# Performance work log

Hardware: AMD Instinct MI355X
Metric: run time of the kernel (lower is better)

Reference implementation:

```python
import jax, jax.numpy as jnp
import numpy as np

B, S, H, F_IN = 256, 128, 512, 1


def _lstm_step(h, c, x, Wih, Whh, b):
    # PyTorch LSTM gate order: i, f, g, o
    gates = x @ Wih.T + h @ Whh.T + b  # (B, 4H)
    i, f, g, o = jnp.split(gates, 4, axis=-1)
    c = jax.nn.sigmoid(f) * c + jax.nn.sigmoid(i) * jnp.tanh(g)
    h = jax.nn.sigmoid(o) * jnp.tanh(c)
    return h, c


def setup_inputs() -> dict:
    key = jax.random.key(0)
    ks = jax.random.split(key, 18)
    p = lambda k, shape: (jax.random.normal(k, shape, dtype=jnp.float32) * 0.05)
    return {
        "input_seq": jax.random.normal(ks[0], (B, S, F_IN), dtype=jnp.float32),
        # encoder: embedding Linear(F_IN -> H) + LSTM(H -> H)
        "We_e": p(ks[1], (H, F_IN)), "be_e": p(ks[2], (H,)),
        "Wih_e": p(ks[3], (4 * H, H)), "Whh_e": p(ks[4], (4 * H, H)), "b_e": p(ks[5], (4 * H,)),
        # decoder: embedding Linear(F_IN -> H) + LSTMCell(H -> H)
        "We_d": p(ks[6], (H, F_IN)), "be_d": p(ks[7], (H,)),
        "Wih_d": p(ks[8], (4 * H, H)), "Whh_d": p(ks[9], (4 * H, H)), "b_d": p(ks[10], (4 * H,)),
        # additive attention: W_1, W_2 (H->H), v (H->1)
        "W1": p(ks[11], (H, H)), "b1": p(ks[12], (H,)),
        "W2": p(ks[13], (H, H)), "b2": p(ks[14], (H,)),
        "v": p(ks[15], (1, H)), "bv": p(ks[16], (1,)),
    }


def reference(input_seq, We_e, be_e, Wih_e, Whh_e, b_e,
              We_d, be_d, Wih_d, Whh_d, b_d,
              W1, b1, W2, b2, v, bv):
    # ---- encoder: embed then LSTM over the sequence ----
    emb = input_seq @ We_e.T + be_e  # (B, S, H)

    def enc_step(carry, x_t):
        h, c = carry
        h, c = _lstm_step(h, c, x_t, Wih_e, Whh_e, b_e)
        return (h, c), h

    h0 = jnp.zeros((B, H), dtype=input_seq.dtype)
    (h, c), enc_h = jax.lax.scan(enc_step, (h0, h0), jnp.swapaxes(emb, 0, 1))
    encoder_output = jnp.swapaxes(enc_h, 0, 1)  # (B, S, H)

    # W_1(encoder_output) is loop-invariant; hoist it (same math as the
    # original, which redundantly recomputes it every step).
    w1enc = encoder_output @ W1.T + b1  # (B, S, H)

    # ---- decoder: per-step LSTMCell + additive attention ----
    def dec_step(carry, _):
        hd, cd, x_in = carry
        e = x_in @ We_d.T + be_d  # (B, H)
        hd, cd = _lstm_step(hd, cd, e, Wih_d, Whh_d, b_d)
        q = hd @ W2.T + b2  # (B, H)
        u = jnp.squeeze(jnp.tanh(w1enc + q[:, None, :]) @ v.T + bv, -1)  # (B, S)
        att = jax.nn.log_softmax(u, axis=1)
        idx = jnp.argmax(att, axis=1)  # pointer (B,)
        # next decoder input = pointed-to input symbol
        x_next = jnp.take_along_axis(input_seq[:, :, 0], idx[:, None], axis=1)  # (B, 1)
        return (hd, cd, x_next), (att, idx)

    x0 = jnp.zeros((B, 1), dtype=input_seq.dtype)
    _, (scores, ptrs) = jax.lax.scan(dec_step, (h, c, x0), None, length=S)
    pointers_scores = jnp.swapaxes(scores, 0, 1)  # (B, S, S) log-probs
    pointers = jnp.swapaxes(ptrs, 0, 1)  # (B, S) int
    return pointers_scores, pointers
```

## Files before the change

### kernel.cpp

```cpp
#include <hip/hip_runtime.h>
#include <hip/hip_fp16.h>

#define Bn 256
#define Sn 128
#define Hn 512
#define G4 2048
#define NBLK 256
#define NTHR 1024
#define HSTR 516
#define LOG2E 1.4426950408889634f

typedef float f4v __attribute__((ext_vector_type(4)));

__device__ __forceinline__ float sigf(float x){
    float e = expf(-fabsf(x));
    float d = 1.f + e;
    return x >= 0.f ? 1.f/d : e/d;
}
__device__ __forceinline__ float ftanh(float x){
    float e = __builtin_amdgcn_exp2f(-2.f * LOG2E * fabsf(x));
    float t = (1.f - e) * __builtin_amdgcn_rcpf(1.f + e);
    return copysignf(t, x);
}

__device__ __forceinline__ float cload(const float* p){
    return __hip_atomic_load((float*)p, __ATOMIC_RELAXED, __HIP_MEMORY_SCOPE_AGENT);
}
__device__ __forceinline__ void cstore(float* p, float v){
    __hip_atomic_store(p, v, __ATOMIC_RELAXED, __HIP_MEMORY_SCOPE_AGENT);
}
__device__ __forceinline__ f4v vload4(const float* p){
    return *(volatile const f4v*)p;
}

__device__ __forceinline__ void gbar(unsigned* slots, unsigned k, int grp){
    __syncthreads();
    if (threadIdx.x < 64) {
        if (threadIdx.x == 0)
            __hip_atomic_store(slots + grp, k, __ATOMIC_RELAXED, __HIP_MEMORY_SCOPE_AGENT);
        unsigned v = (threadIdx.x < 16)
            ? __hip_atomic_load(slots + threadIdx.x, __ATOMIC_RELAXED, __HIP_MEMORY_SCOPE_AGENT)
            : k;
        while (__ballot(v < k)) {
            __builtin_amdgcn_s_sleep(1);
            v = (threadIdx.x < 16)
                ? __hip_atomic_load(slots + threadIdx.x, __ATOMIC_RELAXED, __HIP_MEMORY_SCOPE_AGENT)
                : k;
        }
        asm volatile("" ::: "memory");
    }
    __syncthreads();
}
__device__ __forceinline__ void gbar_sys(unsigned* cnt){
    __syncthreads();
    if (threadIdx.x == 0) {
        __hip_atomic_fetch_add(cnt, 1u, __ATOMIC_RELEASE, __HIP_MEMORY_SCOPE_AGENT);
        while (__hip_atomic_load(cnt, __ATOMIC_RELAXED, __HIP_MEMORY_SCOPE_AGENT) < 16u)
            __builtin_amdgcn_s_sleep(1);
        (void)__hip_atomic_load(cnt, __ATOMIC_ACQUIRE, __HIP_MEMORY_SCOPE_AGENT);
    }
    __syncthreads();
}

__global__ void precompute_kernel(
    const float* __restrict__ Wih_e, const float* __restrict__ We_e,
    const float* __restrict__ be_e,  const float* __restrict__ b_e,
    const float* __restrict__ Wih_d, const float* __restrict__ We_d,
    const float* __restrict__ be_d,  const float* __restrict__ b_d,
    float* __restrict__ p1, float* __restrict__ p0,
    float* __restrict__ r1, float* __restrict__ r0)
{
    int j = blockIdx.x*blockDim.x + threadIdx.x;
    bool dec = j >= G4;
    int jj = dec ? j - G4 : j;
    const float* Wih = dec ? Wih_d : Wih_e;
    const float* We  = dec ? We_d  : We_e;
    const float* be  = dec ? be_d  : be_e;
    const float* bb  = dec ? b_d   : b_e;
    float s1 = 0.f, s0 = 0.f;
    for (int k = 0; k < Hn; ++k) {
        float w = Wih[jj*Hn + k];
        s1 += w * We[k];
        s0 += w * be[k];
    }
    s0 += bb[jj];
    if (dec) { r1[jj] = s1; r0[jj] = s0; }
    else     { p1[jj] = s1; p0[jj] = s0; }
}

__global__ __launch_bounds__(NTHR, 4) void ptrnet_kernel(
    const float* __restrict__ xseq,
    const float* __restrict__ Whh_e, const float* __restrict__ Whh_d,
    const float* __restrict__ W1, const float* __restrict__ b1,
    const float* __restrict__ W2, const float* __restrict__ b2,
    const float* __restrict__ vv,
    const float* __restrict__ p1, const float* __restrict__ p0,
    const float* __restrict__ r1, const float* __restrict__ r0,
    float* __restrict__ hb0, float* __restrict__ hb1,
    float* __restrict__ cbuf, float* __restrict__ qbuf,
    float* __restrict__ x_in, float* __restrict__ w1enc,
    unsigned* __restrict__ barb,
    float* __restrict__ out_scores, float* __restrict__ out_ptr)
{
    __shared__ float smem[16*HSTR + 512*5 + 16];
    float* hs  = smem;
    float* red = smem + 16*HSTR;
    float* qs  = smem;
    float* us  = smem + Hn;
    float* rr  = smem + Hn + Sn + 8;

    const int blk = blockIdx.x;
    const int tid = threadIdx.x;
    const int bt  = blk >> 4, grp = blk & 15;
    const int b0  = bt << 4;
    const int tb  = tid & 15;
    const int hh  = (tid >> 4) & 31;
    const int ks  = tid >> 9;
    const int hg  = (grp << 5) + hh;
    const int kofs = ks << 8;
    unsigned* slots  = barb + bt*64;
    unsigned* syscnt = barb + 1024 + bt*64;
    unsigned bk = 0;
    float* hprev = hb0;
    float* hnext = hb1;

    const int l64 = tid & 63;
    const int kb = l64 << 3;
    float vreg[8];
    #pragma unroll
    for (int j = 0; j < 8; ++j) vreg[j] = vv[kb+j];

#define STAGE_H(SRC) do { \
    for (int i_ = tid; i_ < 16*128; i_ += NTHR) { \
        int r_ = i_ >> 7; int c4_ = (i_ & 127) << 2; \
        *(f4v*)(hs + r_*HSTR + c4_) = vload4((SRC) + (size_t)(b0+r_)*Hn + c4_); \
    } __syncthreads(); } while(0)

    for (int t = 0; t <= Sn; ++t) {
        STAGE_H(hprev);
        float a0=0.f,a1=0.f,a2=0.f,a3=0.f,a4=0.f;
        {
            const float* hrow = hs + tb*HSTR + kofs;
            const float* w0 = Whh_e + (size_t)hg*Hn          + kofs;
            const float* w1r= Whh_e + (size_t)(Hn+hg)*Hn     + kofs;
            const float* w2r= Whh_e + (size_t)(2*Hn+hg)*Hn   + kofs;
            const float* w3r= Whh_e + (size_t)(3*Hn+hg)*Hn   + kofs;
            const float* w4r= W1    + (size_t)hg*Hn          + kofs;
            for (int i = 0; i < 256; i += 4) {
                float4 hv = *(const float4*)(hrow + i);
                float4 x0 = *(const float4*)(w0 + i);
                float4 x1 = *(const float4*)(w1r + i);
                float4 x2 = *(const float4*)(w2r + i);
                float4 x3 = *(const float4*)(w3r + i);
                float4 x4 = *(const float4*)(w4r + i);
                a0 += hv.x*x0.x + hv.y*x0.y + hv.z*x0.z + hv.w*x0.w;
                a1 += hv.x*x1.x + hv.y*x1.y + hv.z*x1.z + hv.w*x1.w;
                a2 += hv.x*x2.x + hv.y*x2.y + hv.z*x2.z + hv.w*x2.w;
                a3 += hv.x*x3.x + hv.y*x3.y + hv.z*x3.z + hv.w*x3.w;
                a4 += hv.x*x4.x + hv.y*x4.y + hv.z*x4.z + hv.w*x4.w;
            }
        }
        if (ks) {
            float* rp = red + (size_t)(tid - 512)*5;
            rp[0]=a0; rp[1]=a1; rp[2]=a2; rp[3]=a3; rp[4]=a4;
        }
        __syncthreads();
        if (!ks) {
            const float* rp = red + (size_t)tid*5;
            a0+=rp[0]; a1+=rp[1]; a2+=rp[2]; a3+=rp[3]; a4+=rp[4];
            size_t off = (size_t)(b0+tb)*Hn + hg;
            if (t < Sn) {
                float xv = xseq[(b0+tb)*Sn + t];
                float gi = a0 + xv*p1[hg]      + p0[hg];
                float gf = a1 + xv*p1[Hn+hg]   + p0[Hn+hg];
                float gg = a2 + xv*p1[2*Hn+hg] + p0[2*Hn+hg];
                float go = a3 + xv*p1[3*Hn+hg] + p0[3*Hn+hg];
                float cn = sigf(gf)*cbuf[off] + sigf(gi)*tanhf(gg);
                float hn = sigf(go)*tanhf(cn);
                cbuf[off] = cn;
                cstore(hnext + off, hn);
            }
            if (t > 0)
                w1enc[((size_t)(b0+tb)*Sn + (t-1))*Hn + hg] = a4 + b1[hg];
        }
        if (t == Sn) gbar_sys(syscnt);
        else         { ++bk; gbar(slots, bk, grp); }
        if (t < Sn) { float* tp = hprev; hprev = hnext; hnext = tp; }
    }

    for (int t = 0; t < Sn; ++t) {
        STAGE_H(hprev);
        float a0=0.f,a1=0.f,a2=0.f,a3=0.f;
        {
            const float* hrow = hs + tb*HSTR + kofs;
            const float* w0 = Whh_d + (size_t)hg*Hn        + kofs;
            const float* w1r= Whh_d + (size_t)(Hn+hg)*Hn   + kofs;
            const float* w2r= Whh_d + (size_t)(2*Hn+hg)*Hn + kofs;
            const float* w3r= Whh_d + (size_t)(3*Hn+hg)*Hn + kofs;
            for (int i = 0; i < 256; i += 4) {
                float4 hv = *(const float4*)(hrow + i);
                float4 x0 = *(const float4*)(w0 + i);
                float4 x1 = *(const float4*)(w1r + i);
                float4 x2 = *(const float4*)(w2r + i);
                float4 x3 = *(const float4*)(w3r + i);
                a0 += hv.x*x0.x + hv.y*x0.y + hv.z*x0.z + hv.w*x0.w;
                a1 += hv.x*x1.x + hv.y*x1.y + hv.z*x1.z + hv.w*x1.w;
                a2 += hv.x*x2.x + hv.y*x2.y + hv.z*x2.z + hv.w*x2.w;
                a3 += hv.x*x3.x + hv.y*x3.y + hv.z*x3.z + hv.w*x3.w;
            }
        }
        if (ks) {
            float* rp = red + (size_t)(tid - 512)*4;
            rp[0]=a0; rp[1]=a1; rp[2]=a2; rp[3]=a3;
        }
        __syncthreads();
        if (!ks) {
            const float* rp = red + (size_t)tid*4;
            a0+=rp[0]; a1+=rp[1]; a2+=rp[2]; a3+=rp[3];
            size_t off = (size_t)(b0+tb)*Hn + hg;
            float xv = cload(x_in + b0 + tb);
            float gi = a0 + xv*r1[hg]      + r0[hg];
            float gf = a1 + xv*r1[Hn+hg]   + r0[Hn+hg];
            float gg = a2 + xv*r1[2*Hn+hg] + r0[2*Hn+hg];
            float go = a3 + xv*r1[3*Hn+hg] + r0[3*Hn+hg];
            float cn = sigf(gf)*cbuf[off] + sigf(gi)*tanhf(gg);
            float hn = sigf(go)*tanhf(cn);
            cbuf[off] = cn;
            cstore(hnext + off, hn);
        }
        ++bk; gbar(slots, bk, grp);
        { float* tp = hprev; hprev = hnext; hnext = tp; }

        STAGE_H(hprev);
        float qa = 0.f;
        {
            const float* hrow = hs + tb*HSTR + kofs;
            const float* wq = W2 + (size_t)hg*Hn + kofs;
            for (int i = 0; i < 256; i += 4) {
                float4 hv = *(const float4*)(hrow + i);
                float4 wv = *(const float4*)(wq + i);
                qa += hv.x*wv.x + hv.y*wv.y + hv.z*wv.z + hv.w*wv.w;
            }
        }
        if (ks) red[tid - 512] = qa;
        __syncthreads();
        if (!ks) cstore(qbuf + (size_t)(b0+tb)*Hn + hg, qa + red[tid] + b2[hg]);
        ++bk; gbar(slots, bk, grp);

        const int b = blk;
        if (tid < 128) {
            f4v q4 = vload4(qbuf + (size_t)b*Hn + (tid << 2));
            *(f4v*)(qs + (tid << 2)) = q4;
        }
        __syncthreads();
        const int wv2 = tid >> 6;
        float qreg[8];
        #pragma unroll
        for (int j = 0; j < 8; ++j) qreg[j] = qs[kb+j];
        #pragma unroll
        for (int si = 0; si < 8; ++si) {
            const int s = (wv2 << 3) + si;
            const float* wr = w1enc + ((size_t)b*Sn + s)*Hn + kb;
            f4v w0 = *(const f4v*)wr;
            f4v w1v = *(const f4v*)(wr + 4);
            float a = 0.f;
            a += vreg[0]*ftanh(w0[0] + qreg[0]);
            a += vreg[1]*ftanh(w0[1] + qreg[1]);
            a += vreg[2]*ftanh(w0[2] + qreg[2]);
            a += vreg[3]*ftanh(w0[3] + qreg[3]);
            a += vreg[4]*ftanh(w1v[0] + qreg[4]);
            a += vreg[5]*ftanh(w1v[1] + qreg[5]);
            a += vreg[6]*ftanh(w1v[2] + qreg[6]);
            a += vreg[7]*ftanh(w1v[3] + qreg[7]);
            a += __shfl_xor(a, 1);  a += __shfl_xor(a, 2);  a += __shfl_xor(a, 4);
            a += __shfl_xor(a, 8);  a += __shfl_xor(a, 16); a += __shfl_xor(a, 32);
            if (l64 == 0) us[s] = a;
        }
        __syncthreads();
        if (tid < 64) {
            float av = us[tid], c2 = us[tid+64];
            float mv; int mi;
            if (c2 > av) { mv = c2; mi = tid+64; } else { mv = av; mi = tid; }
            #pragma unroll
            for (int off2 = 1; off2 < 64; off2 <<= 1) {
                float ov = __shfl_xor(mv, off2);
                int   oi = __shfl_xor(mi, off2);
                if (ov > mv || (ov == mv && oi < mi)) { mv = ov; mi = oi; }
            }
            float es = expf(av - mv) + expf(c2 - mv);
            #pragma unroll
            for (int off2 = 1; off2 < 64; off2 <<= 1) es += __shfl_xor(es, off2);
            if (tid == 0) {
                rr[0] = mv; rr[1] = logf(es);
                out_ptr[b*Sn + t] = (float)mi;
                cstore(x_in + b, xseq[b*Sn + mi]);
            }
        }
        __syncthreads();
        if (tid < Sn)
            out_scores[((size_t)b*Sn + t)*Sn + tid] = us[tid] - rr[0] - rr[1];
        if (t < Sn-1) { ++bk; gbar(slots, bk, grp); }
    }
#undef STAGE_H
}

extern "C" void kernel_launch(void* const* d_in, const int* in_sizes, int n_in,
                              void* d_out, int out_size, void* d_ws, size_t ws_size,
                              hipStream_t stream)
{
    const float* input_seq = (const float*)d_in[0];
    const float* We_e = (const float*)d_in[1],  *be_e = (const float*)d_in[2];
    const float* Wih_e = (const float*)d_in[3], *Whh_e = (const float*)d_in[4];
    const float* b_e = (const float*)d_in[5];
    const float* We_d = (const float*)d_in[6],  *be_d = (const float*)d_in[7];
    const float* Wih_d = (const float*)d_in[8], *Whh_d = (const float*)d_in[9];
    const float* b_d = (const float*)d_in[10];
    const float* W1 = (const float*)d_in[11], *b1 = (const float*)d_in[12];
    const float* W2 = (const float*)d_in[13], *b2 = (const float*)d_in[14];
    const float* v  = (const float*)d_in[15];

    float* ws = (float*)d_ws;
    size_t o = 0;
    float* hb0  = ws + o; o += Bn*Hn;
    float* hb1  = ws + o; o += Bn*Hn;
    float* cbuf = ws + o; o += Bn*Hn;
    float* qbuf = ws + o; o += Bn*Hn;
    float* p1   = ws + o; o += G4;
    float* p0   = ws + o; o += G4;
    float* r1   = ws + o; o += G4;
    float* r0   = ws + o; o += G4;
    float* x_in = ws + o; o += 256;
    unsigned* barb = (unsigned*)(ws + o); o += 2048;
    float* w1enc = ws + o;

    hipMemsetAsync(hb0,  0, Bn*Hn*sizeof(float), stream);
    hipMemsetAsync(cbuf, 0, Bn*Hn*sizeof(float), stream);
    hipMemsetAsync(x_in, 0, (256+2048)*sizeof(float), stream);

    precompute_kernel<<<dim3(16), 256, 0, stream>>>(Wih_e, We_e, be_e, b_e,
                                                    Wih_d, We_d, be_d, b_d,
                                                    p1, p0, r1, r0);

    ptrnet_kernel<<<dim3(NBLK), dim3(NTHR), 0, stream>>>(
        input_seq, Whh_e, Whh_d, W1, b1, W2, b2, v,
        p1, p0, r1, r0, hb0, hb1, cbuf, qbuf, x_in, w1enc, barb,
        (float*)d_out, (float*)d_out + (size_t)Bn*Sn*Sn);
}
```

Before: 12.94 ms.

## Compute decoder query per block locally to drop a grid barrier

Each block now computes the W2 projection of its own batch row's decoder hidden state directly, instead of splitting it across the group and exchanging results through a global q buffer. This removes one grid-wide barrier and the global round-trip for q on every decoder step. In exchange, each block reads all of W2 (1 MB) per step instead of a slice, which raises L2 traffic and adds work on the critical path. The w1enc loads in the attention loop are also software-prefetched one row ahead.

```diff
diff --git a/kernel.cpp b/kernel.cpp
--- a/kernel.cpp
+++ b/kernel.cpp
@@ -97,7 +97,7 @@
     const float* __restrict__ p1, const float* __restrict__ p0,
     const float* __restrict__ r1, const float* __restrict__ r0,
     float* __restrict__ hb0, float* __restrict__ hb1,
-    float* __restrict__ cbuf, float* __restrict__ qbuf,
+    float* __restrict__ cbuf,
     float* __restrict__ x_in, float* __restrict__ w1enc,
     unsigned* __restrict__ barb,
     float* __restrict__ out_scores, float* __restrict__ out_ptr)
@@ -105,9 +105,10 @@
     __shared__ float smem[16*HSTR + 512*5 + 16];
     float* hs  = smem;
     float* red = smem + 16*HSTR;
-    float* qs  = smem;
-    float* us  = smem + Hn;
-    float* rr  = smem + Hn + Sn + 8;
+    float* hds = smem;
+    float* qsf = smem + Hn;
+    float* us  = smem + 2*Hn;
+    float* rr  = smem + 2*Hn + Sn + 8;
 
     const int blk = blockIdx.x;
     const int tid = threadIdx.x;
@@ -231,38 +232,46 @@
         ++bk; gbar(slots, bk, grp);
         { float* tp = hprev; hprev = hnext; hnext = tp; }
 
-        STAGE_H(hprev);
-        float qa = 0.f;
+        const int b = blk;
+        if (tid < 128)
+            *(f4v*)(hds + (tid << 2)) = vload4(hprev + (size_t)b*Hn + (tid << 2));
+        __syncthreads();
         {
-            const float* hrow = hs + tb*HSTR + kofs;
-            const float* wq = W2 + (size_t)hg*Hn + kofs;
-            for (int i = 0; i < 256; i += 4) {
-                float4 hv = *(const float4*)(hrow + i);
-                float4 wv = *(const float4*)(wq + i);
-                qa += hv.x*wv.x + hv.y*wv.y + hv.z*wv.z + hv.w*wv.w;
-            }
-        }
-        if (ks) red[tid - 512] = qa;
-        __syncthreads();
-        if (!ks) cstore(qbuf + (size_t)(b0+tb)*Hn + hg, qa + red[tid] + b2[hg]);
-        ++bk; gbar(slots, bk, grp);
-
-        const int b = blk;
-        if (tid < 128) {
-            f4v q4 = vload4(qbuf + (size_t)b*Hn + (tid << 2));
-            *(f4v*)(qs + (tid << 2)) = q4;
+            const int nl = tid >> 3;
+            const int k8 = tid & 7;
+            const float* hdp = hds + (k8 << 6);
+            #pragma unroll
+            for (int c = 0; c < 4; ++c) {
+                const int n = (c << 7) + nl;
+                const float* wr2 = W2 + (size_t)n*Hn + (k8 << 6);
+                float acc = 0.f;
+                for (int i = 0; i < 64; i += 4) {
+                    float4 wv = *(const float4*)(wr2 + i);
+                    acc += hdp[i]*wv.x + hdp[i+1]*wv.y
+                         + hdp[i+2]*wv.z + hdp[i+3]*wv.w;
+                }
+                acc += __shfl_xor(acc, 1);
+                acc += __shfl_xor(acc, 2);
+                acc += __shfl_xor(acc, 4);
+                if (k8 == 0) qsf[n] = acc + b2[n];
+            }
         }
         __syncthreads();
         const int wv2 = tid >> 6;
         float qreg[8];
         #pragma unroll
-        for (int j = 0; j < 8; ++j) qreg[j] = qs[kb+j];
+        for (int j = 0; j < 8; ++j) qreg[j] = qsf[kb+j];
+        const float* wbase = w1enc + ((size_t)b*Sn + (wv2 << 3))*Hn + kb;
+        f4v w0 = *(const f4v*)wbase;
+        f4v w1v = *(const f4v*)(wbase + 4);
         #pragma unroll
         for (int si = 0; si < 8; ++si) {
-            const int s = (wv2 << 3) + si;
-            const float* wr = w1enc + ((size_t)b*Sn + s)*Hn + kb;
-            f4v w0 = *(const f4v*)wr;
-            f4v w1v = *(const f4v*)(wr + 4);
+            f4v n0 = w0, n1 = w1v;
+            if (si < 7) {
+                const float* wr = wbase + (size_t)(si+1)*Hn;
+                n0 = *(const f4v*)wr;
+                n1 = *(const f4v*)(wr + 4);
+            }
             float a = 0.f;
             a += vreg[0]*ftanh(w0[0] + qreg[0]);
             a += vreg[1]*ftanh(w0[1] + qreg[1]);
@@ -274,7 +283,8 @@
             a += vreg[7]*ftanh(w1v[3] + qreg[7]);
             a += __shfl_xor(a, 1);  a += __shfl_xor(a, 2);  a += __shfl_xor(a, 4);
             a += __shfl_xor(a, 8);  a += __shfl_xor(a, 16); a += __shfl_xor(a, 32);
-            if (l64 == 0) us[s] = a;
+            if (l64 == 0) us[(wv2 << 3) + si] = a;
+            w0 = n0; w1v = n1;
         }
         __syncthreads();
         if (tid < 64) {
@@ -324,7 +334,6 @@
     float* hb0  = ws + o; o += Bn*Hn;
     float* hb1  = ws + o; o += Bn*Hn;
     float* cbuf = ws + o; o += Bn*Hn;
-    float* qbuf = ws + o; o += Bn*Hn;
     float* p1   = ws + o; o += G4;
     float* p0   = ws + o; o += G4;
     float* r1   = ws + o; o += G4;
@@ -343,6 +352,6 @@
 
     ptrnet_kernel<<<dim3(NBLK), dim3(NTHR), 0, stream>>>(
         input_seq, Whh_e, Whh_d, W1, b1, W2, b2, v,
-        p1, p0, r1, r0, hb0, hb1, cbuf, qbuf, x_in, w1enc, barb,
+        p1, p0, r1, r0, hb0, hb1, cbuf, x_in, w1enc, barb,
         (float*)d_out, (float*)d_out + (size_t)Bn*Sn*Sn);
 }
```

Result: slower. 15.45 ms (+19.4%).
